# Kernel tuning notes

Measured on AMD Instinct MI355X. Metric: run time of the kernel, lower is better.

The kernel has to match this reference:

```python
import jax, jax.numpy as jnp
import numpy as np
from jax import lax

P = 2048
HIDDEN = 512
NUM_STEPS = 15
BATCH = 8192
SLOPE = 25.0  # snntorch surrogate.fast_sigmoid default slope


@jax.custom_vjp
def spike_fn(x):
    # Heaviside forward, fast-sigmoid surrogate backward.
    return (x > 0).astype(x.dtype)

def _spike_fwd(x):
    return spike_fn(x), x

def _spike_bwd(x, g):
    return (g / (SLOPE * jnp.abs(x) + 1.0) ** 2,)

spike_fn.defvjp(_spike_fwd, _spike_bwd)


def setup_inputs() -> dict:
    key = jax.random.key(0)
    ks = jax.random.split(key, 6)
    x = jax.random.randint(ks[0], (BATCH, 2), 0, P)
    embed = jax.random.normal(ks[1], (P, HIDDEN), dtype=jnp.float32)
    # Linear weights stored [in, out] (transpose of torch convention, same math)
    W1 = jax.random.normal(ks[2], (2 * HIDDEN, HIDDEN), dtype=jnp.float32) * (1.0 / np.sqrt(2 * HIDDEN))
    b1 = jnp.zeros((HIDDEN,), dtype=jnp.float32)
    W2 = jax.random.normal(ks[3], (HIDDEN, P), dtype=jnp.float32) * (1.0 / np.sqrt(HIDDEN))
    b2 = jnp.zeros((P,), dtype=jnp.float32)
    beta1 = jnp.float32(0.9)
    thr1 = jnp.float32(1.0)
    beta2 = jnp.float32(0.9)
    thr2 = jnp.float32(1.0)
    return {"x": x, "embed": embed, "W1": W1, "b1": b1, "W2": W2, "b2": b2,
            "beta1": beta1, "thr1": thr1, "beta2": beta2, "thr2": thr2}


def reference(x, embed, W1, b1, W2, b2, beta1, thr1, beta2, thr2):
    # clamp params as in the torch no-grad block (identity at init values)
    beta1 = jnp.clip(beta1, 0.1, 0.9)
    beta2 = jnp.clip(beta2, 0.1, 0.9)
    thr1 = jnp.clip(thr1, 0.1, None)
    thr2 = jnp.clip(thr2, 0.1, None)

    emb = embed[x].reshape(x.shape[0], -1)          # [B, 2*hidden]
    cur1 = emb @ W1 + b1                            # constant across steps

    mem1_0 = jnp.zeros((x.shape[0], HIDDEN), dtype=jnp.float32)
    mem2_0 = jnp.zeros((x.shape[0], P), dtype=jnp.float32)

    def step(carry, _):
        mem1, mem2 = carry
        # snntorch Leaky, reset_mechanism='subtract': reset from PREVIOUS mem, detached
        reset1 = lax.stop_gradient((mem1 - thr1 > 0).astype(mem1.dtype))
        mem1 = beta1 * mem1 + cur1 - reset1 * thr1
        spk1 = spike_fn(mem1 - thr1)
        cur2 = spk1 @ W2 + b2
        # lif2 has reset_mechanism='none'
        mem2 = beta2 * mem2 + cur2
        return (mem1, mem2), None

    (mem1, mem2), _ = lax.scan(step, (mem1_0, mem2_0), None, length=NUM_STEPS)
    return mem2  # output = last mem2
```

## Files before the change

### kernel.cpp

```cpp
#include <hip/hip_runtime.h>
#include <hip/hip_bf16.h>
#include <stdint.h>

typedef float    f32x4 __attribute__((ext_vector_type(4)));
typedef _Float16 f16x4 __attribute__((ext_vector_type(4)));
typedef _Float16 f16x8 __attribute__((ext_vector_type(8)));

#define NSTEPS 15

__global__ __launch_bounds__(256) void prep_kernel(
    const float* __restrict__ embed, const float* __restrict__ W1,
    const float* __restrict__ W2, const float* __restrict__ b2,
    const float* __restrict__ beta2p,
    _Float16* __restrict__ Ap, _Float16* __restrict__ Btp,
    _Float16* __restrict__ W2T, float* __restrict__ bias2s)
{
  __shared__ _Float16 sh[2][64][72];
  const int b = blockIdx.x;
  const int t = threadIdx.x;

  if (b < 1024) {
    const int i  = b * 256 + t;
    const int m  = i >> 7;
    const int k4 = (i & 127) * 4;
    f32x4 v = *(const f32x4*)&embed[(size_t)m * 512 + k4];
    f16x4 h0, h1;
#pragma unroll
    for (int j = 0; j < 4; ++j) {
      h0[j] = (_Float16)v[j];
      h1[j] = (_Float16)(v[j] - (float)h0[j]);
    }
    _Float16* r = Ap + (size_t)m * 1024 + k4;
    *(f16x4*)(r)       = h0;
    *(f16x4*)(r + 512) = h1;
  } else if (b < 1152) {
    const int idx = b - 1024;
    const int n0 = (idx & 7) * 64;
    const int k0 = ((idx >> 3) & 7) * 64;
    const int z  = idx >> 6;
    const int kk = t >> 4;
    const int n4 = (t & 15) * 4;
#pragma unroll
    for (int i = 0; i < 4; ++i) {
      f32x4 v = *(const f32x4*)&W1[(size_t)(z * 512 + k0 + kk + i * 16) * 512 + n0 + n4];
#pragma unroll
      for (int j = 0; j < 4; ++j) {
        float s = v[j] * 64.0f;
        _Float16 hi = (_Float16)s;
        sh[0][n4 + j][kk + i * 16] = hi;
        sh[1][n4 + j][kk + i * 16] = (_Float16)(s - (float)hi);
      }
    }
    __syncthreads();
#pragma unroll
    for (int i = 0; i < 2; ++i) {
      const int nn = (t >> 3) + i * 32;
      const int k8 = (t & 7) * 8;
      _Float16* r = Btp + (size_t)(z * 512 + n0 + nn) * 1024 + k0 + k8;
      *(uint4*)(r)       = *(const uint4*)&sh[0][nn][k8];
      *(uint4*)(r + 512) = *(const uint4*)&sh[1][nn][k8];
    }
  } else if (b < 1408) {
    const int idx = b - 1152;
    const int n0 = (idx & 31) * 64;
    const int k0 = (idx >> 5) * 64;
    const int kk = t >> 4;
    const int n4 = (t & 15) * 4;
#pragma unroll
    for (int i = 0; i < 4; ++i) {
      f32x4 v = *(const f32x4*)&W2[(size_t)(k0 + kk + i * 16) * 2048 + n0 + n4];
#pragma unroll
      for (int j = 0; j < 4; ++j) sh[0][n4 + j][kk + i * 16] = (_Float16)v[j];
    }
    __syncthreads();
#pragma unroll
    for (int i = 0; i < 2; ++i) {
      const int nn = (t >> 3) + i * 32;
      const int k8 = (t & 7) * 8;
      *(uint4*)&W2T[(size_t)(n0 + nn) * 512 + k0 + k8] = *(const uint4*)&sh[0][nn][k8];
    }
  } else {
    const float beta2 = fminf(fmaxf(beta2p[0], 0.1f), 0.9f);
    float cb = 0.0f;
    for (int i = 0; i < NSTEPS; ++i) cb = beta2 * cb + 1.0f;
    const int n = (b - 1408) * 256 + t;
    if (n < 2048) bias2s[n] = cb * b2[n];
  }
}

__device__ __forceinline__ void gld_lds16(const void* g, void* l) {
  __builtin_amdgcn_global_load_lds(
      (const __attribute__((address_space(1))) uint32_t*)g,
      (__attribute__((address_space(3))) uint32_t*)l, 16, 0, 0);
}

__global__ __launch_bounds__(256) void gemm1_kernel(
    const _Float16* __restrict__ Ap,
    const _Float16* __restrict__ Btp,
    float* __restrict__ Tp)
{
  __shared__ __align__(16) char lds[(128 + 64) * 128];
  char* AsB = lds;
  char* BsB = lds + 128 * 128;

  const int t    = threadIdx.x;
  const int lane = t & 63;
  const int wave = t >> 6;
  const int z    = blockIdx.y;

  int bid = blockIdx.x;
  bid = (bid & 7) * 32 + (bid >> 3);
  const int m0 = (bid >> 4) * 128;
  const int n0 = (bid & 15) * 64;

  f32x4 acc[2][4] = {};

  for (int kt = 0; kt < 12; ++kt) {
    const int k0   = z * 768 + kt * 64;
    const int acol = (k0 < 1024) ? k0 : k0 - 1024;
    const int bcol = (k0 < 1024) ? (k0 & 511) : k0 - 512;
#pragma unroll
    for (int i = 0; i < 4; ++i) {
      const int ob  = i * 4096 + wave * 1024;
      const int o   = ob + lane * 16;
      const int row = o >> 7;
      const int c   = ((o >> 4) & 7) ^ (row & 7);
      gld_lds16(Ap + ((size_t)(m0 + row) * 1024 + acol + c * 8), AsB + ob);
    }
#pragma unroll
    for (int i = 0; i < 2; ++i) {
      const int ob  = i * 4096 + wave * 1024;
      const int o   = ob + lane * 16;
      const int row = o >> 7;
      const int c   = ((o >> 4) & 7) ^ (row & 7);
      gld_lds16(Btp + ((size_t)(n0 + row) * 1024 + bcol + c * 8), BsB + ob);
    }
    asm volatile("s_waitcnt vmcnt(0)" ::: "memory");
    __syncthreads();

#pragma unroll
    for (int kk = 0; kk < 2; ++kk) {
      const int lc = (lane >> 4) + kk * 4;
      f16x8 af[2], bf[4];
#pragma unroll
      for (int mi = 0; mi < 2; ++mi) {
        const int row = wave * 32 + mi * 16 + (lane & 15);
        af[mi] = *(const f16x8*)(AsB + row * 128 + ((lc ^ (row & 7)) << 4));
      }
#pragma unroll
      for (int ni = 0; ni < 4; ++ni) {
        const int row = ni * 16 + (lane & 15);
        bf[ni] = *(const f16x8*)(BsB + row * 128 + ((lc ^ (row & 7)) << 4));
      }
#pragma unroll
      for (int mi = 0; mi < 2; ++mi)
#pragma unroll
        for (int ni = 0; ni < 4; ++ni)
          acc[mi][ni] = __builtin_amdgcn_mfma_f32_16x16x32_f16(
              af[mi], bf[ni], acc[mi][ni], 0, 0, 0);
    }
    __syncthreads();
  }

  float* Cz = Tp + (size_t)z * 2048 * 1024;
#pragma unroll
  for (int mi = 0; mi < 2; ++mi) {
    const int r0 = m0 + wave * 32 + mi * 16 + ((lane >> 4) << 2);
#pragma unroll
    for (int ni = 0; ni < 4; ++ni) {
      const int cc = n0 + ni * 16 + (lane & 15);
#pragma unroll
      for (int q = 0; q < 4; ++q)
        Cz[(size_t)(r0 + q) * 1024 + cc] = acc[mi][ni][q] * 0.015625f;
    }
  }
}

__global__ __launch_bounds__(256) void recur_kernel(
    const int* __restrict__ x,
    const float* __restrict__ Tp,
    const float* __restrict__ b1,
    const float* __restrict__ beta1p, const float* __restrict__ thr1p,
    const float* __restrict__ beta2p,
    _Float16* __restrict__ S)
{
  const float beta1 = fminf(fmaxf(beta1p[0], 0.1f), 0.9f);
  const float thr1  = fmaxf(thr1p[0], 0.1f);
  const float beta2 = fminf(fmaxf(beta2p[0], 0.1f), 0.9f);
  const size_t ZS = (size_t)2048 * 1024;

  const int t = threadIdx.x;
  const int b = blockIdx.x * 4 + (t >> 6);
  const int h = (t & 63) * 8;
  const int x0 = x[b * 2 + 0];
  const int x1 = x[b * 2 + 1];

  const float* p00 = &Tp[(size_t)x0 * 1024 + h];
  const float* p01 = &Tp[(size_t)x1 * 1024 + 512 + h];

  float cur[8];
#pragma unroll
  for (int half = 0; half < 2; ++half) {
    f32x4 a0 = *(const f32x4*)(p00 + half * 4);
    f32x4 a1 = *(const f32x4*)(p00 + ZS + half * 4);
    f32x4 c0 = *(const f32x4*)(p01 + half * 4);
    f32x4 c1 = *(const f32x4*)(p01 + ZS + half * 4);
    f32x4 e  = *(const f32x4*)&b1[h + half * 4];
#pragma unroll
    for (int j = 0; j < 4; ++j)
      cur[half * 4 + j] = (a0[j] + a1[j]) + (c0[j] + c1[j]) + e[j];
  }

  float m[8] = {}, s[8] = {};
#pragma unroll
  for (int st = 0; st < NSTEPS; ++st) {
#pragma unroll
    for (int j = 0; j < 8; ++j) {
      float r = (m[j] > thr1) ? thr1 : 0.0f;
      m[j] = beta1 * m[j] + cur[j] - r;
      float sp = (m[j] > thr1) ? 1.0f : 0.0f;
      s[j] = beta2 * s[j] + sp;
    }
  }

  __align__(16) _Float16 o[8];
#pragma unroll
  for (int j = 0; j < 8; ++j) o[j] = (_Float16)s[j];
  *(uint4*)&S[(size_t)b * 512 + h] = *(const uint4*)o;
}

template<int BM, int BN, int WM_, int WN_, int LDA, int LDB, int LDC,
         int KTILES, int NTN, bool BIAS>
__global__ __launch_bounds__(256) void mfma_gemm_kernel(
    const _Float16* __restrict__ A, const _Float16* __restrict__ Bt,
    const float* __restrict__ bias, float* __restrict__ C, float scale)
{
  constexpr int FM  = BM / (WM_ * 16);
  constexpr int FN  = BN / (WN_ * 16);
  constexpr int ITA = BM / 32;
  constexpr int ITB = BN / 32;

  __shared__ __align__(16) char lds[BM * 128 + BN * 128];
  char* AsB = lds;
  char* BsB = lds + BM * 128;

  const int t    = threadIdx.x;
  const int lane = t & 63;
  const int wave = t >> 6;
  const int wm   = wave / WN_;
  const int wn   = wave % WN_;

  int bid = blockIdx.x;
  bid = (bid & 7) * (gridDim.x >> 3) + (bid >> 3);
  const int m0 = (bid / NTN) * BM;
  const int n0 = (bid % NTN) * BN;

  f32x4 acc[FM][FN] = {};

  for (int kt = 0; kt < KTILES; ++kt) {
    const int k0 = kt * 64;
#pragma unroll
    for (int i = 0; i < ITA; ++i) {
      const int ob  = i * 4096 + wave * 1024;
      const int o   = ob + lane * 16;
      const int row = o >> 7;
      const int c   = ((o >> 4) & 7) ^ (row & 7);
      gld_lds16(A + ((size_t)(m0 + row) * LDA + k0 + c * 8), AsB + ob);
    }
#pragma unroll
    for (int i = 0; i < ITB; ++i) {
      const int ob  = i * 4096 + wave * 1024;
      const int o   = ob + lane * 16;
      const int row = o >> 7;
      const int c   = ((o >> 4) & 7) ^ (row & 7);
      gld_lds16(Bt + ((size_t)(n0 + row) * LDB + k0 + c * 8), BsB + ob);
    }
    asm volatile("s_waitcnt vmcnt(0)" ::: "memory");
    __syncthreads();

#pragma unroll
    for (int kk = 0; kk < 2; ++kk) {
      const int lc = (lane >> 4) + kk * 4;
      f16x8 af[FM], bf[FN];
#pragma unroll
      for (int mi = 0; mi < FM; ++mi) {
        const int row = wm * (FM * 16) + mi * 16 + (lane & 15);
        af[mi] = *(const f16x8*)(AsB + row * 128 + ((lc ^ (row & 7)) << 4));
      }
#pragma unroll
      for (int ni = 0; ni < FN; ++ni) {
        const int row = wn * (FN * 16) + ni * 16 + (lane & 15);
        bf[ni] = *(const f16x8*)(BsB + row * 128 + ((lc ^ (row & 7)) << 4));
      }
#pragma unroll
      for (int mi = 0; mi < FM; ++mi)
#pragma unroll
        for (int ni = 0; ni < FN; ++ni)
          acc[mi][ni] = __builtin_amdgcn_mfma_f32_16x16x32_f16(
              af[mi], bf[ni], acc[mi][ni], 0, 0, 0);
    }
    __syncthreads();
  }

#pragma unroll
  for (int mi = 0; mi < FM; ++mi) {
    const int r0 = m0 + wm * (FM * 16) + mi * 16 + ((lane >> 4) << 2);
#pragma unroll
    for (int ni = 0; ni < FN; ++ni) {
      const int cc = n0 + wn * (FN * 16) + ni * 16 + (lane & 15);
      const float bv = BIAS ? bias[cc] : 0.0f;
#pragma unroll
      for (int q = 0; q < 4; ++q)
        C[(size_t)(r0 + q) * LDC + cc] = acc[mi][ni][q] * scale + bv;
    }
  }
}

extern "C" void kernel_launch(void* const* d_in, const int* in_sizes, int n_in,
                              void* d_out, int out_size, void* d_ws, size_t ws_size,
                              hipStream_t stream) {
  const int*   x     = (const int*)  d_in[0];
  const float* embed = (const float*)d_in[1];
  const float* W1    = (const float*)d_in[2];
  const float* b1    = (const float*)d_in[3];
  const float* W2    = (const float*)d_in[4];
  const float* b2    = (const float*)d_in[5];
  const float* beta1 = (const float*)d_in[6];
  const float* thr1  = (const float*)d_in[7];
  const float* beta2 = (const float*)d_in[8];
  float* out = (float*)d_out;

  char* ws = (char*)d_ws;
  float*    Tp     = (float*)   ws;
  _Float16* Ap     = (_Float16*)(ws + (16u << 20));
  _Float16* Btp    = (_Float16*)(ws + (20u << 20));
  _Float16* W2T    = (_Float16*)(ws + (22u << 20));
  _Float16* S      = (_Float16*)(ws + (24u << 20));
  float*    bias2s = (float*)   (ws + (32u << 20));

  prep_kernel<<<dim3(1416), 256, 0, stream>>>(embed, W1, W2, b2, beta2,
                                              Ap, Btp, W2T, bias2s);

  gemm1_kernel<<<dim3(256, 2), 256, 0, stream>>>(Ap, Btp, Tp);

  recur_kernel<<<dim3(2048), 256, 0, stream>>>(x, Tp, b1, beta1, thr1, beta2, S);

  mfma_gemm_kernel<128, 128, 2, 2, 512, 512, 2048, 8, 16, true>
      <<<dim3(1024), 256, 0, stream>>>(S, W2T, bias2s, out, 1.0f);
}
```

Measured before the change: 65.71 us.

## Replace output GEMM with triple-buffered 256x128 pipelined MFMA kernel

Replaces the simple single-buffered 128x128 output GEMM with a 512-thread kernel using 256x128 tiles. It triple-buffers LDS and interleaves global-to-LDS prefetch of tile k+2 with MFMA work on tile k, using split waitcnts, barriers and s_setprio. The aim is to hide global load latency and cut the full-drain syncs per K step. In exchange it uses 144KB of LDS per block, which limits occupancy, and relies on fragile hand-placed waitcnt accounting.

```diff
diff --git a/kernel.cpp b/kernel.cpp
--- a/kernel.cpp
+++ b/kernel.cpp
@@ -229,89 +229,142 @@
   *(uint4*)&S[(size_t)b * 512 + h] = *(const uint4*)o;
 }
 
-template<int BM, int BN, int WM_, int WN_, int LDA, int LDB, int LDC,
-         int KTILES, int NTN, bool BIAS>
-__global__ __launch_bounds__(256) void mfma_gemm_kernel(
+__device__ __forceinline__ void g2_round(
     const _Float16* __restrict__ A, const _Float16* __restrict__ Bt,
-    const float* __restrict__ bias, float* __restrict__ C, float scale)
-{
-  constexpr int FM  = BM / (WM_ * 16);
-  constexpr int FN  = BN / (WN_ * 16);
-  constexpr int ITA = BM / 32;
-  constexpr int ITB = BN / 32;
-
-  __shared__ __align__(16) char lds[BM * 128 + BN * 128];
-  char* AsB = lds;
-  char* BsB = lds + BM * 128;
+    char* lds, int m0, int n0, int wave, int lane, int tile, int r)
+{
+  const int k0 = tile * 64;
+  char* lb = lds + (tile % 3) * 49152;
+  if (r < 4) {
+    const int ob  = r * 8192 + wave * 1024;
+    const int o   = ob + lane * 16;
+    const int row = o >> 7;
+    const int c   = ((o >> 4) & 7) ^ (row & 7);
+    gld_lds16(A + ((size_t)(m0 + row) * 512 + k0 + c * 8), lb + ob);
+  } else {
+    const int ob  = (r - 4) * 8192 + wave * 1024;
+    const int o   = ob + lane * 16;
+    const int row = o >> 7;
+    const int c   = ((o >> 4) & 7) ^ (row & 7);
+    gld_lds16(Bt + ((size_t)(n0 + row) * 512 + k0 + c * 8), lb + 32768 + ob);
+  }
+}
+
+template<int QA>
+__device__ __forceinline__ void g2_mfma16(
+    f32x4 (&acc)[8][2], const f16x8 (&af)[4][2], const f16x8 (&bf)[2][2])
+{
+#pragma unroll
+  for (int kk = 0; kk < 2; ++kk)
+#pragma unroll
+    for (int mi = 0; mi < 4; ++mi)
+#pragma unroll
+      for (int ni = 0; ni < 2; ++ni)
+        acc[QA * 4 + mi][ni] = __builtin_amdgcn_mfma_f32_16x16x32_f16(
+            af[mi][kk], bf[ni][kk], acc[QA * 4 + mi][ni], 0, 0, 0);
+}
+
+template<int QA>
+__device__ __forceinline__ void g2_lda(
+    f16x8 (&af)[4][2], const char* lb, int wm, int lane)
+{
+#pragma unroll
+  for (int mi = 0; mi < 4; ++mi) {
+    const int row = wm * 128 + QA * 64 + mi * 16 + (lane & 15);
+#pragma unroll
+    for (int kk = 0; kk < 2; ++kk) {
+      const int lc = (lane >> 4) + kk * 4;
+      af[mi][kk] = *(const f16x8*)(lb + row * 128 + ((lc ^ (row & 7)) << 4));
+    }
+  }
+}
+
+__device__ __forceinline__ void g2_ldb(
+    f16x8 (&bf)[2][2], const char* lb, int wn, int lane)
+{
+#pragma unroll
+  for (int ni = 0; ni < 2; ++ni) {
+    const int row = wn * 32 + ni * 16 + (lane & 15);
+#pragma unroll
+    for (int kk = 0; kk < 2; ++kk) {
+      const int lc = (lane >> 4) + kk * 4;
+      bf[ni][kk] = *(const f16x8*)(lb + 32768 + row * 128 + ((lc ^ (row & 7)) << 4));
+    }
+  }
+}
+
+__global__ __launch_bounds__(512, 2) void gemm2_pipe_kernel(
+    const _Float16* __restrict__ A,
+    const _Float16* __restrict__ Bt,
+    const float* __restrict__ bias,
+    float* __restrict__ C)
+{
+  __shared__ __align__(16) char lds[3 * 49152];
 
   const int t    = threadIdx.x;
   const int lane = t & 63;
   const int wave = t >> 6;
-  const int wm   = wave / WN_;
-  const int wn   = wave % WN_;
+  const int wm   = wave >> 2;
+  const int wn   = wave & 3;
 
   int bid = blockIdx.x;
-  bid = (bid & 7) * (gridDim.x >> 3) + (bid >> 3);
-  const int m0 = (bid / NTN) * BM;
-  const int n0 = (bid % NTN) * BN;
-
-  f32x4 acc[FM][FN] = {};
-
-  for (int kt = 0; kt < KTILES; ++kt) {
-    const int k0 = kt * 64;
-#pragma unroll
-    for (int i = 0; i < ITA; ++i) {
-      const int ob  = i * 4096 + wave * 1024;
-      const int o   = ob + lane * 16;
-      const int row = o >> 7;
-      const int c   = ((o >> 4) & 7) ^ (row & 7);
-      gld_lds16(A + ((size_t)(m0 + row) * LDA + k0 + c * 8), AsB + ob);
-    }
-#pragma unroll
-    for (int i = 0; i < ITB; ++i) {
-      const int ob  = i * 4096 + wave * 1024;
-      const int o   = ob + lane * 16;
-      const int row = o >> 7;
-      const int c   = ((o >> 4) & 7) ^ (row & 7);
-      gld_lds16(Bt + ((size_t)(n0 + row) * LDB + k0 + c * 8), BsB + ob);
-    }
-    asm volatile("s_waitcnt vmcnt(0)" ::: "memory");
-    __syncthreads();
-
-#pragma unroll
-    for (int kk = 0; kk < 2; ++kk) {
-      const int lc = (lane >> 4) + kk * 4;
-      f16x8 af[FM], bf[FN];
-#pragma unroll
-      for (int mi = 0; mi < FM; ++mi) {
-        const int row = wm * (FM * 16) + mi * 16 + (lane & 15);
-        af[mi] = *(const f16x8*)(AsB + row * 128 + ((lc ^ (row & 7)) << 4));
-      }
-#pragma unroll
-      for (int ni = 0; ni < FN; ++ni) {
-        const int row = wn * (FN * 16) + ni * 16 + (lane & 15);
-        bf[ni] = *(const f16x8*)(BsB + row * 128 + ((lc ^ (row & 7)) << 4));
-      }
-#pragma unroll
-      for (int mi = 0; mi < FM; ++mi)
-#pragma unroll
-        for (int ni = 0; ni < FN; ++ni)
-          acc[mi][ni] = __builtin_amdgcn_mfma_f32_16x16x32_f16(
-              af[mi], bf[ni], acc[mi][ni], 0, 0, 0);
-    }
-    __syncthreads();
-  }
-
-#pragma unroll
-  for (int mi = 0; mi < FM; ++mi) {
-    const int r0 = m0 + wm * (FM * 16) + mi * 16 + ((lane >> 4) << 2);
-#pragma unroll
-    for (int ni = 0; ni < FN; ++ni) {
-      const int cc = n0 + wn * (FN * 16) + ni * 16 + (lane & 15);
-      const float bv = BIAS ? bias[cc] : 0.0f;
+  bid = (bid & 7) * 64 + (bid >> 3);
+  const int m0 = (bid >> 4) * 256;
+  const int n0 = (bid & 15) * 128;
+
+  f32x4 acc[8][2] = {};
+  f16x8 af[4][2], bf[2][2];
+
+#pragma unroll
+  for (int r = 0; r < 6; ++r) g2_round(A, Bt, lds, m0, n0, wave, lane, 0, r);
+#pragma unroll
+  for (int r = 0; r < 6; ++r) g2_round(A, Bt, lds, m0, n0, wave, lane, 1, r);
+  asm volatile("s_waitcnt vmcnt(6)" ::: "memory");
+  __builtin_amdgcn_s_barrier();
+
+  for (int tt = 0; tt < 8; ++tt) {
+    const char* lb = lds + (tt % 3) * 49152;
+    const bool pf = (tt + 2 < 8);
+
+    g2_lda<0>(af, lb, wm, lane);
+    g2_ldb(bf, lb, wn, lane);
+    if (pf) {
+      g2_round(A, Bt, lds, m0, n0, wave, lane, tt + 2, 0);
+      g2_round(A, Bt, lds, m0, n0, wave, lane, tt + 2, 1);
+      g2_round(A, Bt, lds, m0, n0, wave, lane, tt + 2, 2);
+    }
+    __builtin_amdgcn_s_barrier();
+    asm volatile("s_waitcnt lgkmcnt(0)" ::: "memory");
+    __builtin_amdgcn_s_setprio(1);
+    g2_mfma16<0>(acc, af, bf);
+    __builtin_amdgcn_s_setprio(0);
+    __builtin_amdgcn_s_barrier();
+
+    g2_lda<1>(af, lb, wm, lane);
+    if (pf) {
+      g2_round(A, Bt, lds, m0, n0, wave, lane, tt + 2, 3);
+      g2_round(A, Bt, lds, m0, n0, wave, lane, tt + 2, 4);
+      g2_round(A, Bt, lds, m0, n0, wave, lane, tt + 2, 5);
+    }
+    __builtin_amdgcn_s_barrier();
+    asm volatile("s_waitcnt lgkmcnt(0)" ::: "memory");
+    __builtin_amdgcn_s_setprio(1);
+    g2_mfma16<1>(acc, af, bf);
+    __builtin_amdgcn_s_setprio(0);
+    asm volatile("s_waitcnt vmcnt(6)" ::: "memory");
+    __builtin_amdgcn_s_barrier();
+  }
+
+#pragma unroll
+  for (int a = 0; a < 8; ++a) {
+    const int r0 = m0 + wm * 128 + a * 16 + ((lane >> 4) << 2);
+#pragma unroll
+    for (int ni = 0; ni < 2; ++ni) {
+      const int cc = n0 + wn * 32 + ni * 16 + (lane & 15);
+      const float bv = bias[cc];
 #pragma unroll
       for (int q = 0; q < 4; ++q)
-        C[(size_t)(r0 + q) * LDC + cc] = acc[mi][ni][q] * scale + bv;
+        C[(size_t)(r0 + q) * 2048 + cc] = acc[a][ni][q] + bv;
     }
   }
 }
@@ -345,6 +398,5 @@
 
   recur_kernel<<<dim3(2048), 256, 0, stream>>>(x, Tp, b1, beta1, thr1, beta2, S);
 
-  mfma_gemm_kernel<128, 128, 2, 2, 512, 512, 2048, 8, 16, true>
-      <<<dim3(1024), 256, 0, stream>>>(S, W2T, bias2s, out, 1.0f);
-}
+  gemm2_pipe_kernel<<<dim3(512), 512, 0, stream>>>(S, W2T, bias2s, out);
+}
```

After: 65.23 us. No clear change (-0.7%).

## Fuse four launches into a persistent megakernel with grid-wide barriers

Applied to the files above, without the earlier changes.

Replaces the prep, gemm1, recurrence and output GEMM launches with a single persistent 256-block kernel that separates the phases with atomic-counter grid barriers, removing inter-kernel launch gaps. The final GEMM now uses 256x256 tiles with double-buffered LDS prefetch and wave priority hints, and folds the bias scaling into its epilogue. The risks are barrier spin overhead, possible deadlock if not all blocks are co-resident, and lower parallelism in the earlier phases with only 256 blocks.

```diff
diff --git a/kernel.cpp b/kernel.cpp
--- a/kernel.cpp
+++ b/kernel.cpp
@@ -7,86 +7,7 @@
 typedef _Float16 f16x8 __attribute__((ext_vector_type(8)));
 
 #define NSTEPS 15
-
-__global__ __launch_bounds__(256) void prep_kernel(
-    const float* __restrict__ embed, const float* __restrict__ W1,
-    const float* __restrict__ W2, const float* __restrict__ b2,
-    const float* __restrict__ beta2p,
-    _Float16* __restrict__ Ap, _Float16* __restrict__ Btp,
-    _Float16* __restrict__ W2T, float* __restrict__ bias2s)
-{
-  __shared__ _Float16 sh[2][64][72];
-  const int b = blockIdx.x;
-  const int t = threadIdx.x;
-
-  if (b < 1024) {
-    const int i  = b * 256 + t;
-    const int m  = i >> 7;
-    const int k4 = (i & 127) * 4;
-    f32x4 v = *(const f32x4*)&embed[(size_t)m * 512 + k4];
-    f16x4 h0, h1;
-#pragma unroll
-    for (int j = 0; j < 4; ++j) {
-      h0[j] = (_Float16)v[j];
-      h1[j] = (_Float16)(v[j] - (float)h0[j]);
-    }
-    _Float16* r = Ap + (size_t)m * 1024 + k4;
-    *(f16x4*)(r)       = h0;
-    *(f16x4*)(r + 512) = h1;
-  } else if (b < 1152) {
-    const int idx = b - 1024;
-    const int n0 = (idx & 7) * 64;
-    const int k0 = ((idx >> 3) & 7) * 64;
-    const int z  = idx >> 6;
-    const int kk = t >> 4;
-    const int n4 = (t & 15) * 4;
-#pragma unroll
-    for (int i = 0; i < 4; ++i) {
-      f32x4 v = *(const f32x4*)&W1[(size_t)(z * 512 + k0 + kk + i * 16) * 512 + n0 + n4];
-#pragma unroll
-      for (int j = 0; j < 4; ++j) {
-        float s = v[j] * 64.0f;
-        _Float16 hi = (_Float16)s;
-        sh[0][n4 + j][kk + i * 16] = hi;
-        sh[1][n4 + j][kk + i * 16] = (_Float16)(s - (float)hi);
-      }
-    }
-    __syncthreads();
-#pragma unroll
-    for (int i = 0; i < 2; ++i) {
-      const int nn = (t >> 3) + i * 32;
-      const int k8 = (t & 7) * 8;
-      _Float16* r = Btp + (size_t)(z * 512 + n0 + nn) * 1024 + k0 + k8;
-      *(uint4*)(r)       = *(const uint4*)&sh[0][nn][k8];
-      *(uint4*)(r + 512) = *(const uint4*)&sh[1][nn][k8];
-    }
-  } else if (b < 1408) {
-    const int idx = b - 1152;
-    const int n0 = (idx & 31) * 64;
-    const int k0 = (idx >> 5) * 64;
-    const int kk = t >> 4;
-    const int n4 = (t & 15) * 4;
-#pragma unroll
-    for (int i = 0; i < 4; ++i) {
-      f32x4 v = *(const f32x4*)&W2[(size_t)(k0 + kk + i * 16) * 2048 + n0 + n4];
-#pragma unroll
-      for (int j = 0; j < 4; ++j) sh[0][n4 + j][kk + i * 16] = (_Float16)v[j];
-    }
-    __syncthreads();
-#pragma unroll
-    for (int i = 0; i < 2; ++i) {
-      const int nn = (t >> 3) + i * 32;
-      const int k8 = (t & 7) * 8;
-      *(uint4*)&W2T[(size_t)(n0 + nn) * 512 + k0 + k8] = *(const uint4*)&sh[0][nn][k8];
-    }
-  } else {
-    const float beta2 = fminf(fmaxf(beta2p[0], 0.1f), 0.9f);
-    float cb = 0.0f;
-    for (int i = 0; i < NSTEPS; ++i) cb = beta2 * cb + 1.0f;
-    const int n = (b - 1408) * 256 + t;
-    if (n < 2048) bias2s[n] = cb * b2[n];
-  }
-}
+#define NBLK 256u
 
 __device__ __forceinline__ void gld_lds16(const void* g, void* l) {
   __builtin_amdgcn_global_load_lds(
@@ -94,224 +15,341 @@
       (__attribute__((address_space(3))) uint32_t*)l, 16, 0, 0);
 }
 
-__global__ __launch_bounds__(256) void gemm1_kernel(
-    const _Float16* __restrict__ Ap,
-    const _Float16* __restrict__ Btp,
-    float* __restrict__ Tp)
+__device__ __forceinline__ void gbar(unsigned* c) {
+  __syncthreads();
+  if (threadIdx.x == 0) {
+    __threadfence();
+    __hip_atomic_fetch_add(c, 1u, __ATOMIC_ACQ_REL, __HIP_MEMORY_SCOPE_AGENT);
+    while (__hip_atomic_load(c, __ATOMIC_ACQUIRE, __HIP_MEMORY_SCOPE_AGENT) < NBLK)
+      __builtin_amdgcn_s_sleep(2);
+  }
+  __syncthreads();
+}
+
+__global__ void init_kernel(unsigned* cnt) {
+  if (threadIdx.x < 8) cnt[threadIdx.x] = 0u;
+}
+
+__global__ __launch_bounds__(512, 2) void mega_kernel(
+    const int* __restrict__ x, const float* __restrict__ embed,
+    const float* __restrict__ W1, const float* __restrict__ b1,
+    const float* __restrict__ W2, const float* __restrict__ b2,
+    const float* __restrict__ beta1p, const float* __restrict__ thr1p,
+    const float* __restrict__ beta2p,
+    _Float16* __restrict__ Ap, _Float16* __restrict__ Btp,
+    _Float16* __restrict__ W2T, float* __restrict__ Tp,
+    _Float16* __restrict__ S, unsigned* __restrict__ cnt,
+    float* __restrict__ out)
 {
-  __shared__ __align__(16) char lds[(128 + 64) * 128];
-  char* AsB = lds;
-  char* BsB = lds + 128 * 128;
-
+  __shared__ __align__(16) char lds[131072];
   const int t    = threadIdx.x;
+  const int b    = blockIdx.x;
   const int lane = t & 63;
   const int wave = t >> 6;
-  const int z    = blockIdx.y;
-
-  int bid = blockIdx.x;
-  bid = (bid & 7) * 32 + (bid >> 3);
-  const int m0 = (bid >> 4) * 128;
-  const int n0 = (bid & 15) * 64;
-
-  f32x4 acc[2][4] = {};
-
-  for (int kt = 0; kt < 12; ++kt) {
-    const int k0   = z * 768 + kt * 64;
-    const int acol = (k0 < 1024) ? k0 : k0 - 1024;
-    const int bcol = (k0 < 1024) ? (k0 & 511) : k0 - 512;
-#pragma unroll
-    for (int i = 0; i < 4; ++i) {
-      const int ob  = i * 4096 + wave * 1024;
+
+  {
+#pragma unroll
+    for (int pass = 0; pass < 2; ++pass) {
+      const int i  = pass * 131072 + b * 512 + t;
+      const int m  = i >> 7;
+      const int k4 = (i & 127) * 4;
+      f32x4 v = *(const f32x4*)&embed[(size_t)m * 512 + k4];
+      f16x4 h0, h1;
+#pragma unroll
+      for (int j = 0; j < 4; ++j) {
+        h0[j] = (_Float16)v[j];
+        h1[j] = (_Float16)(v[j] - (float)h0[j]);
+      }
+      _Float16* r = Ap + (size_t)m * 1024 + k4;
+      *(f16x4*)(r)       = h0;
+      *(f16x4*)(r + 512) = h1;
+    }
+
+    auto sh = (_Float16(*)[2][64][72])lds;
+    const int half = t >> 8;
+    const int tq   = t & 255;
+    const int kk   = tq >> 4;
+    const int n4   = (tq & 15) * 4;
+
+    if (b < 64) {
+      const int v  = b * 2 + half;
+      const int n0 = (v & 7) * 64;
+      const int k0 = ((v >> 3) & 7) * 64;
+      const int z  = v >> 6;
+#pragma unroll
+      for (int i = 0; i < 4; ++i) {
+        f32x4 w = *(const f32x4*)&W1[(size_t)(z * 512 + k0 + kk + i * 16) * 512 + n0 + n4];
+#pragma unroll
+        for (int j = 0; j < 4; ++j) {
+          float s = w[j] * 64.0f;
+          _Float16 hi = (_Float16)s;
+          sh[half][0][n4 + j][kk + i * 16] = hi;
+          sh[half][1][n4 + j][kk + i * 16] = (_Float16)(s - (float)hi);
+        }
+      }
+    } else if (b < 192) {
+      const int v  = (b - 64) * 2 + half;
+      const int n0 = (v & 31) * 64;
+      const int k0 = (v >> 5) * 64;
+#pragma unroll
+      for (int i = 0; i < 4; ++i) {
+        f32x4 w = *(const f32x4*)&W2[(size_t)(k0 + kk + i * 16) * 2048 + n0 + n4];
+#pragma unroll
+        for (int j = 0; j < 4; ++j) sh[half][0][n4 + j][kk + i * 16] = (_Float16)w[j];
+      }
+    }
+    __syncthreads();
+    if (b < 64) {
+      const int v  = b * 2 + half;
+      const int n0 = (v & 7) * 64;
+      const int k0 = ((v >> 3) & 7) * 64;
+      const int z  = v >> 6;
+#pragma unroll
+      for (int i = 0; i < 2; ++i) {
+        const int nn = (tq >> 3) + i * 32;
+        const int k8 = (tq & 7) * 8;
+        _Float16* r = Btp + (size_t)(z * 512 + n0 + nn) * 1024 + k0 + k8;
+        *(uint4*)(r)       = *(const uint4*)&sh[half][0][nn][k8];
+        *(uint4*)(r + 512) = *(const uint4*)&sh[half][1][nn][k8];
+      }
+    } else if (b < 192) {
+      const int v  = (b - 64) * 2 + half;
+      const int n0 = (v & 31) * 64;
+      const int k0 = (v >> 5) * 64;
+#pragma unroll
+      for (int i = 0; i < 2; ++i) {
+        const int nn = (tq >> 3) + i * 32;
+        const int k8 = (tq & 7) * 8;
+        *(uint4*)&W2T[(size_t)(n0 + nn) * 512 + k0 + k8] = *(const uint4*)&sh[half][0][nn][k8];
+      }
+    }
+  }
+  gbar(cnt + 0);
+
+  {
+    const int z  = wave >> 2;
+    const int vw = wave & 3;
+    char* AsB = lds + z * 24576;
+    char* BsB = AsB + 16384;
+
+    const int bid = (b & 7) * 32 + (b >> 3);
+    const int m0 = (bid >> 4) * 128;
+    const int n0 = (bid & 15) * 64;
+
+    f32x4 acc[2][4] = {};
+
+    for (int kt = 0; kt < 12; ++kt) {
+      const int vk0  = z * 768 + kt * 64;
+      const int acol = (vk0 < 1024) ? vk0 : vk0 - 1024;
+      const int bcol = (vk0 < 1024) ? (vk0 & 511) : vk0 - 512;
+#pragma unroll
+      for (int i = 0; i < 4; ++i) {
+        const int ob  = i * 4096 + vw * 1024;
+        const int o   = ob + lane * 16;
+        const int row = o >> 7;
+        const int c   = ((o >> 4) & 7) ^ (row & 7);
+        gld_lds16(Ap + ((size_t)(m0 + row) * 1024 + acol + c * 8), AsB + ob);
+      }
+#pragma unroll
+      for (int i = 0; i < 2; ++i) {
+        const int ob  = i * 4096 + vw * 1024;
+        const int o   = ob + lane * 16;
+        const int row = o >> 7;
+        const int c   = ((o >> 4) & 7) ^ (row & 7);
+        gld_lds16(Btp + ((size_t)(n0 + row) * 1024 + bcol + c * 8), BsB + ob);
+      }
+      asm volatile("s_waitcnt vmcnt(0)" ::: "memory");
+      __syncthreads();
+
+#pragma unroll
+      for (int kk = 0; kk < 2; ++kk) {
+        const int lc = (lane >> 4) + kk * 4;
+        f16x8 af[2], bf[4];
+#pragma unroll
+        for (int mi = 0; mi < 2; ++mi) {
+          const int row = vw * 32 + mi * 16 + (lane & 15);
+          af[mi] = *(const f16x8*)(AsB + row * 128 + ((lc ^ (row & 7)) << 4));
+        }
+#pragma unroll
+        for (int ni = 0; ni < 4; ++ni) {
+          const int row = ni * 16 + (lane & 15);
+          bf[ni] = *(const f16x8*)(BsB + row * 128 + ((lc ^ (row & 7)) << 4));
+        }
+#pragma unroll
+        for (int mi = 0; mi < 2; ++mi)
+#pragma unroll
+          for (int ni = 0; ni < 4; ++ni)
+            acc[mi][ni] = __builtin_amdgcn_mfma_f32_16x16x32_f16(
+                af[mi], bf[ni], acc[mi][ni], 0, 0, 0);
+      }
+      __syncthreads();
+    }
+
+    float* Cz = Tp + (size_t)z * 2048 * 1024;
+#pragma unroll
+    for (int mi = 0; mi < 2; ++mi) {
+      const int r0 = m0 + vw * 32 + mi * 16 + ((lane >> 4) << 2);
+#pragma unroll
+      for (int ni = 0; ni < 4; ++ni) {
+        const int cc = n0 + ni * 16 + (lane & 15);
+#pragma unroll
+        for (int q = 0; q < 4; ++q)
+          Cz[(size_t)(r0 + q) * 1024 + cc] = acc[mi][ni][q] * 0.015625f;
+      }
+    }
+  }
+  gbar(cnt + 1);
+
+  {
+    const float beta1 = fminf(fmaxf(beta1p[0], 0.1f), 0.9f);
+    const float thr1  = fmaxf(thr1p[0], 0.1f);
+    const float beta2 = fminf(fmaxf(beta2p[0], 0.1f), 0.9f);
+    const size_t ZS = (size_t)2048 * 1024;
+    const int h = (t & 63) * 8;
+
+#pragma unroll
+    for (int pass = 0; pass < 4; ++pass) {
+      const int bs = b * 32 + pass * 8 + (t >> 6);
+      const int x0 = x[bs * 2 + 0];
+      const int x1 = x[bs * 2 + 1];
+      const float* p0 = &Tp[(size_t)x0 * 1024 + h];
+      const float* p1 = &Tp[(size_t)x1 * 1024 + 512 + h];
+
+      float cur[8];
+#pragma unroll
+      for (int half = 0; half < 2; ++half) {
+        f32x4 a0 = *(const f32x4*)(p0 + half * 4);
+        f32x4 a1 = *(const f32x4*)(p0 + ZS + half * 4);
+        f32x4 c0 = *(const f32x4*)(p1 + half * 4);
+        f32x4 c1 = *(const f32x4*)(p1 + ZS + half * 4);
+        f32x4 e  = *(const f32x4*)&b1[h + half * 4];
+#pragma unroll
+        for (int j = 0; j < 4; ++j)
+          cur[half * 4 + j] = (a0[j] + a1[j]) + (c0[j] + c1[j]) + e[j];
+      }
+
+      float m[8] = {}, s[8] = {};
+#pragma unroll
+      for (int st = 0; st < NSTEPS; ++st) {
+#pragma unroll
+        for (int j = 0; j < 8; ++j) {
+          float r = (m[j] > thr1) ? thr1 : 0.0f;
+          m[j] = beta1 * m[j] + cur[j] - r;
+          float sp = (m[j] > thr1) ? 1.0f : 0.0f;
+          s[j] = beta2 * s[j] + sp;
+        }
+      }
+      __align__(16) _Float16 o[8];
+#pragma unroll
+      for (int j = 0; j < 8; ++j) o[j] = (_Float16)s[j];
+      *(uint4*)&S[(size_t)bs * 512 + h] = *(const uint4*)o;
+    }
+  }
+  gbar(cnt + 2);
+
+  {
+    const int wm = wave >> 2;
+    const int wn = wave & 3;
+    const int bid = (b & 7) * 32 + (b >> 3);
+    const int m0 = (bid >> 3) * 256;
+    const int n0 = (bid & 7) * 256;
+
+    f32x4 acc[8][4] = {};
+
+    auto stage = [&](int tile, int r) {
+      const int k0  = tile * 64;
+      char* slot    = lds + (tile & 1) * 65536;
+      const int ob  = (r & 3) * 8192 + wave * 1024;
       const int o   = ob + lane * 16;
       const int row = o >> 7;
       const int c   = ((o >> 4) & 7) ^ (row & 7);
-      gld_lds16(Ap + ((size_t)(m0 + row) * 1024 + acol + c * 8), AsB + ob);
-    }
-#pragma unroll
-    for (int i = 0; i < 2; ++i) {
-      const int ob  = i * 4096 + wave * 1024;
-      const int o   = ob + lane * 16;
-      const int row = o >> 7;
-      const int c   = ((o >> 4) & 7) ^ (row & 7);
-      gld_lds16(Btp + ((size_t)(n0 + row) * 1024 + bcol + c * 8), BsB + ob);
-    }
+      if (r < 4)
+        gld_lds16(S   + ((size_t)(m0 + row) * 512 + k0 + c * 8), slot + ob);
+      else
+        gld_lds16(W2T + ((size_t)(n0 + row) * 512 + k0 + c * 8), slot + 32768 + ob);
+    };
+
+#pragma unroll
+    for (int r = 0; r < 8; ++r) stage(0, r);
     asm volatile("s_waitcnt vmcnt(0)" ::: "memory");
     __syncthreads();
 
-#pragma unroll
-    for (int kk = 0; kk < 2; ++kk) {
-      const int lc = (lane >> 4) + kk * 4;
-      f16x8 af[2], bf[4];
-#pragma unroll
-      for (int mi = 0; mi < 2; ++mi) {
-        const int row = wave * 32 + mi * 16 + (lane & 15);
-        af[mi] = *(const f16x8*)(AsB + row * 128 + ((lc ^ (row & 7)) << 4));
-      }
+    f16x8 bf[4][2];
+    for (int tt = 0; tt < 8; ++tt) {
+      const char* lb = lds + (tt & 1) * 65536;
+      const bool pf = (tt < 7);
+
 #pragma unroll
       for (int ni = 0; ni < 4; ++ni) {
-        const int row = ni * 16 + (lane & 15);
-        bf[ni] = *(const f16x8*)(BsB + row * 128 + ((lc ^ (row & 7)) << 4));
-      }
-#pragma unroll
-      for (int mi = 0; mi < 2; ++mi)
-#pragma unroll
-        for (int ni = 0; ni < 4; ++ni)
-          acc[mi][ni] = __builtin_amdgcn_mfma_f32_16x16x32_f16(
-              af[mi], bf[ni], acc[mi][ni], 0, 0, 0);
-    }
-    __syncthreads();
-  }
-
-  float* Cz = Tp + (size_t)z * 2048 * 1024;
-#pragma unroll
-  for (int mi = 0; mi < 2; ++mi) {
-    const int r0 = m0 + wave * 32 + mi * 16 + ((lane >> 4) << 2);
-#pragma unroll
-    for (int ni = 0; ni < 4; ++ni) {
-      const int cc = n0 + ni * 16 + (lane & 15);
-#pragma unroll
-      for (int q = 0; q < 4; ++q)
-        Cz[(size_t)(r0 + q) * 1024 + cc] = acc[mi][ni][q] * 0.015625f;
-    }
-  }
-}
-
-__global__ __launch_bounds__(256) void recur_kernel(
-    const int* __restrict__ x,
-    const float* __restrict__ Tp,
-    const float* __restrict__ b1,
-    const float* __restrict__ beta1p, const float* __restrict__ thr1p,
-    const float* __restrict__ beta2p,
-    _Float16* __restrict__ S)
-{
-  const float beta1 = fminf(fmaxf(beta1p[0], 0.1f), 0.9f);
-  const float thr1  = fmaxf(thr1p[0], 0.1f);
-  const float beta2 = fminf(fmaxf(beta2p[0], 0.1f), 0.9f);
-  const size_t ZS = (size_t)2048 * 1024;
-
-  const int t = threadIdx.x;
-  const int b = blockIdx.x * 4 + (t >> 6);
-  const int h = (t & 63) * 8;
-  const int x0 = x[b * 2 + 0];
-  const int x1 = x[b * 2 + 1];
-
-  const float* p00 = &Tp[(size_t)x0 * 1024 + h];
-  const float* p01 = &Tp[(size_t)x1 * 1024 + 512 + h];
-
-  float cur[8];
-#pragma unroll
-  for (int half = 0; half < 2; ++half) {
-    f32x4 a0 = *(const f32x4*)(p00 + half * 4);
-    f32x4 a1 = *(const f32x4*)(p00 + ZS + half * 4);
-    f32x4 c0 = *(const f32x4*)(p01 + half * 4);
-    f32x4 c1 = *(const f32x4*)(p01 + ZS + half * 4);
-    f32x4 e  = *(const f32x4*)&b1[h + half * 4];
-#pragma unroll
-    for (int j = 0; j < 4; ++j)
-      cur[half * 4 + j] = (a0[j] + a1[j]) + (c0[j] + c1[j]) + e[j];
-  }
-
-  float m[8] = {}, s[8] = {};
-#pragma unroll
-  for (int st = 0; st < NSTEPS; ++st) {
-#pragma unroll
-    for (int j = 0; j < 8; ++j) {
-      float r = (m[j] > thr1) ? thr1 : 0.0f;
-      m[j] = beta1 * m[j] + cur[j] - r;
-      float sp = (m[j] > thr1) ? 1.0f : 0.0f;
-      s[j] = beta2 * s[j] + sp;
-    }
-  }
-
-  __align__(16) _Float16 o[8];
-#pragma unroll
-  for (int j = 0; j < 8; ++j) o[j] = (_Float16)s[j];
-  *(uint4*)&S[(size_t)b * 512 + h] = *(const uint4*)o;
-}
-
-template<int BM, int BN, int WM_, int WN_, int LDA, int LDB, int LDC,
-         int KTILES, int NTN, bool BIAS>
-__global__ __launch_bounds__(256) void mfma_gemm_kernel(
-    const _Float16* __restrict__ A, const _Float16* __restrict__ Bt,
-    const float* __restrict__ bias, float* __restrict__ C, float scale)
-{
-  constexpr int FM  = BM / (WM_ * 16);
-  constexpr int FN  = BN / (WN_ * 16);
-  constexpr int ITA = BM / 32;
-  constexpr int ITB = BN / 32;
-
-  __shared__ __align__(16) char lds[BM * 128 + BN * 128];
-  char* AsB = lds;
-  char* BsB = lds + BM * 128;
-
-  const int t    = threadIdx.x;
-  const int lane = t & 63;
-  const int wave = t >> 6;
-  const int wm   = wave / WN_;
-  const int wn   = wave % WN_;
-
-  int bid = blockIdx.x;
-  bid = (bid & 7) * (gridDim.x >> 3) + (bid >> 3);
-  const int m0 = (bid / NTN) * BM;
-  const int n0 = (bid % NTN) * BN;
-
-  f32x4 acc[FM][FN] = {};
-
-  for (int kt = 0; kt < KTILES; ++kt) {
-    const int k0 = kt * 64;
-#pragma unroll
-    for (int i = 0; i < ITA; ++i) {
-      const int ob  = i * 4096 + wave * 1024;
-      const int o   = ob + lane * 16;
-      const int row = o >> 7;
-      const int c   = ((o >> 4) & 7) ^ (row & 7);
-      gld_lds16(A + ((size_t)(m0 + row) * LDA + k0 + c * 8), AsB + ob);
-    }
-#pragma unroll
-    for (int i = 0; i < ITB; ++i) {
-      const int ob  = i * 4096 + wave * 1024;
-      const int o   = ob + lane * 16;
-      const int row = o >> 7;
-      const int c   = ((o >> 4) & 7) ^ (row & 7);
-      gld_lds16(Bt + ((size_t)(n0 + row) * LDB + k0 + c * 8), BsB + ob);
-    }
-    asm volatile("s_waitcnt vmcnt(0)" ::: "memory");
-    __syncthreads();
-
-#pragma unroll
-    for (int kk = 0; kk < 2; ++kk) {
-      const int lc = (lane >> 4) + kk * 4;
-      f16x8 af[FM], bf[FN];
-#pragma unroll
-      for (int mi = 0; mi < FM; ++mi) {
-        const int row = wm * (FM * 16) + mi * 16 + (lane & 15);
-        af[mi] = *(const f16x8*)(AsB + row * 128 + ((lc ^ (row & 7)) << 4));
-      }
-#pragma unroll
-      for (int ni = 0; ni < FN; ++ni) {
-        const int row = wn * (FN * 16) + ni * 16 + (lane & 15);
-        bf[ni] = *(const f16x8*)(BsB + row * 128 + ((lc ^ (row & 7)) << 4));
-      }
-#pragma unroll
-      for (int mi = 0; mi < FM; ++mi)
-#pragma unroll
-        for (int ni = 0; ni < FN; ++ni)
-          acc[mi][ni] = __builtin_amdgcn_mfma_f32_16x16x32_f16(
-              af[mi], bf[ni], acc[mi][ni], 0, 0, 0);
-    }
-    __syncthreads();
-  }
-
-#pragma unroll
-  for (int mi = 0; mi < FM; ++mi) {
-    const int r0 = m0 + wm * (FM * 16) + mi * 16 + ((lane >> 4) << 2);
-#pragma unroll
-    for (int ni = 0; ni < FN; ++ni) {
-      const int cc = n0 + wn * (FN * 16) + ni * 16 + (lane & 15);
-      const float bv = BIAS ? bias[cc] : 0.0f;
-#pragma unroll
-      for (int q = 0; q < 4; ++q)
-        C[(size_t)(r0 + q) * LDC + cc] = acc[mi][ni][q] * scale + bv;
+        const int row = wn * 64 + ni * 16 + (lane & 15);
+#pragma unroll
+        for (int kk = 0; kk < 2; ++kk) {
+          const int lc = (lane >> 4) + kk * 4;
+          bf[ni][kk] = *(const f16x8*)(lb + 32768 + row * 128 + ((lc ^ (row & 7)) << 4));
+        }
+      }
+      f16x8 af[4][2];
+#pragma unroll
+      for (int mi = 0; mi < 4; ++mi) {
+        const int row = wm * 128 + mi * 16 + (lane & 15);
+#pragma unroll
+        for (int kk = 0; kk < 2; ++kk) {
+          const int lc = (lane >> 4) + kk * 4;
+          af[mi][kk] = *(const f16x8*)(lb + row * 128 + ((lc ^ (row & 7)) << 4));
+        }
+      }
+      if (pf) { stage(tt + 1, 0); stage(tt + 1, 1); stage(tt + 1, 2); stage(tt + 1, 3); }
+      __builtin_amdgcn_s_setprio(1);
+#pragma unroll
+      for (int kk = 0; kk < 2; ++kk)
+#pragma unroll
+        for (int mi = 0; mi < 4; ++mi)
+#pragma unroll
+          for (int ni = 0; ni < 4; ++ni)
+            acc[mi][ni] = __builtin_amdgcn_mfma_f32_16x16x32_f16(
+                af[mi][kk], bf[ni][kk], acc[mi][ni], 0, 0, 0);
+      __builtin_amdgcn_s_setprio(0);
+
+#pragma unroll
+      for (int mi = 0; mi < 4; ++mi) {
+        const int row = wm * 128 + 64 + mi * 16 + (lane & 15);
+#pragma unroll
+        for (int kk = 0; kk < 2; ++kk) {
+          const int lc = (lane >> 4) + kk * 4;
+          af[mi][kk] = *(const f16x8*)(lb + row * 128 + ((lc ^ (row & 7)) << 4));
+        }
+      }
+      if (pf) { stage(tt + 1, 4); stage(tt + 1, 5); stage(tt + 1, 6); stage(tt + 1, 7); }
+      __builtin_amdgcn_s_setprio(1);
+#pragma unroll
+      for (int kk = 0; kk < 2; ++kk)
+#pragma unroll
+        for (int mi = 0; mi < 4; ++mi)
+#pragma unroll
+          for (int ni = 0; ni < 4; ++ni)
+            acc[4 + mi][ni] = __builtin_amdgcn_mfma_f32_16x16x32_f16(
+                af[mi][kk], bf[ni][kk], acc[4 + mi][ni], 0, 0, 0);
+      __builtin_amdgcn_s_setprio(0);
+
+      asm volatile("s_waitcnt vmcnt(0)" ::: "memory");
+      __syncthreads();
+    }
+
+    const float beta2 = fminf(fmaxf(beta2p[0], 0.1f), 0.9f);
+    float cb = 0.0f;
+    for (int i = 0; i < NSTEPS; ++i) cb = beta2 * cb + 1.0f;
+
+#pragma unroll
+    for (int a = 0; a < 8; ++a) {
+      const int r0 = m0 + wm * 128 + (a >> 2) * 64 + (a & 3) * 16 + ((lane >> 4) << 2);
+#pragma unroll
+      for (int ni = 0; ni < 4; ++ni) {
+        const int cc = n0 + wn * 64 + ni * 16 + (lane & 15);
+        const float bv = cb * b2[cc];
+#pragma unroll
+        for (int q = 0; q < 4; ++q)
+          out[(size_t)(r0 + q) * 2048 + cc] = acc[a][ni][q] + bv;
+      }
     }
   }
 }
@@ -331,20 +369,15 @@
   float* out = (float*)d_out;
 
   char* ws = (char*)d_ws;
-  float*    Tp     = (float*)   ws;
-  _Float16* Ap     = (_Float16*)(ws + (16u << 20));
-  _Float16* Btp    = (_Float16*)(ws + (20u << 20));
-  _Float16* W2T    = (_Float16*)(ws + (22u << 20));
-  _Float16* S      = (_Float16*)(ws + (24u << 20));
-  float*    bias2s = (float*)   (ws + (32u << 20));
-
-  prep_kernel<<<dim3(1416), 256, 0, stream>>>(embed, W1, W2, b2, beta2,
-                                              Ap, Btp, W2T, bias2s);
-
-  gemm1_kernel<<<dim3(256, 2), 256, 0, stream>>>(Ap, Btp, Tp);
-
-  recur_kernel<<<dim3(2048), 256, 0, stream>>>(x, Tp, b1, beta1, thr1, beta2, S);
-
-  mfma_gemm_kernel<128, 128, 2, 2, 512, 512, 2048, 8, 16, true>
-      <<<dim3(1024), 256, 0, stream>>>(S, W2T, bias2s, out, 1.0f);
-}
+  float*    Tp  = (float*)   ws;
+  _Float16* Ap  = (_Float16*)(ws + (16u << 20));
+  _Float16* Btp = (_Float16*)(ws + (20u << 20));
+  _Float16* W2T = (_Float16*)(ws + (22u << 20));
+  _Float16* S   = (_Float16*)(ws + (24u << 20));
+  unsigned* cnt = (unsigned*)(ws + (32u << 20));
+
+  init_kernel<<<dim3(1), 64, 0, stream>>>(cnt);
+  mega_kernel<<<dim3(256), 512, 0, stream>>>(
+      x, embed, W1, b1, W2, b2, beta1, thr1, beta2,
+      Ap, Btp, W2T, Tp, S, cnt, out);
+}
```

Result: slower. 147.0 us (+123.7%).
